# Kernel tuning notes

Measured on AMD Instinct MI355X. Metric: run time of the kernel, lower is better.

Reference implementation:

```python
import jax, jax.numpy as jnp
import numpy as np

INPUT_DIM = 20000
UNITS = 4096
NNZ = 800000
BATCH = 1024


def setup_inputs() -> dict:
    key = jax.random.key(0)
    k1, k2, k3, k4 = jax.random.split(key, 4)
    x = jax.random.normal(k1, (BATCH, INPUT_DIM), dtype=jnp.float32)
    kernel_vector = jax.random.normal(k2, (NNZ,), dtype=jnp.float32) * 0.05
    bias = jnp.zeros((UNITS,), dtype=jnp.float32)
    rows = jax.random.randint(k3, (NNZ,), 0, INPUT_DIM, dtype=jnp.int32)
    cols = jax.random.randint(k4, (NNZ,), 0, UNITS, dtype=jnp.int32)
    nonzero_ind = jnp.stack([rows, cols], axis=1)  # [NNZ, 2]
    return {"x": x, "kernel_vector": kernel_vector, "bias": bias, "nonzero_ind": nonzero_ind}


def reference(x, kernel_vector, bias, nonzero_ind):
    # scatter_nd: build dense (input_dim, units) kernel; duplicates accumulate (matches tf.scatter_nd)
    input_dim = x.shape[1]
    units = bias.shape[0]
    dense_kernel = jnp.zeros((input_dim, units), dtype=kernel_vector.dtype)
    dense_kernel = dense_kernel.at[nonzero_ind[:, 0], nonzero_ind[:, 1]].add(kernel_vector)
    out = jnp.matmul(x, dense_kernel) + bias  # [B, units]
    return jnp.tanh(out)
```

## Files before the change

### kernel.cpp

```cpp
#include <hip/hip_runtime.h>
#include <hip/hip_fp16.h>

#define BATCH      1024
#define INPUT_DIM  20000
#define UNITS      4096
#define NNZ        800000
#define SLOT_CAP   384

#define WS_XT     0
#define WS_CNT    40960000
#define WS_PACKED (WS_CNT + 16384)

__global__ void transpose_in_kernel(const float* __restrict__ x,
                                    unsigned short* __restrict__ xT,
                                    int* __restrict__ cnt) {
    int flat = blockIdx.y * gridDim.x + blockIdx.x;
    int gid = flat * 256 + threadIdx.y * 32 + threadIdx.x;
    if (gid < UNITS) cnt[gid] = 0;

    __shared__ float tile[32][33];
    int d0 = blockIdx.x * 32;
    int b0 = blockIdx.y * 32;
    int tx = threadIdx.x, ty = threadIdx.y;
#pragma unroll
    for (int i = 0; i < 32; i += 8)
        tile[ty + i][tx] = x[(size_t)(b0 + ty + i) * INPUT_DIM + d0 + tx];
    __syncthreads();
#pragma unroll
    for (int i = 0; i < 32; i += 8) {
        __half h = __float2half(tile[tx][ty + i]);
        xT[(size_t)(d0 + ty + i) * BATCH + b0 + tx] = __half_as_ushort(h);
    }
}

__global__ void scatter_kernel(const int* __restrict__ ind, const float* __restrict__ vals,
                               int* __restrict__ cnt, unsigned int* __restrict__ packed) {
    int i = blockIdx.x * blockDim.x + threadIdx.x;
    if (i < NNZ) {
        int r = ind[2 * i];
        int c = ind[2 * i + 1];
        unsigned short hv = __half_as_ushort(__float2half(vals[i]));
        unsigned int e = (unsigned int)r | ((unsigned int)hv << 16);
        int pos = atomicAdd(&cnt[c], 1);
        if (pos < SLOT_CAP) packed[c * SLOT_CAP + pos] = e;
    }
}

__device__ __forceinline__ void acc_one(unsigned int e, const unsigned short* xb,
                                        float& a0, float& a1) {
    unsigned int row = e & 0xFFFFu;
    __half v = __ushort_as_half((unsigned short)(e >> 16));
    unsigned int q = *(const unsigned int*)(xb + ((size_t)row << 10));
    __half2 h = *(__half2*)&q;
    a0 = fmaf(__half2float(__low2half(h)),  __half2float(v), a0);
    a1 = fmaf(__half2float(__high2half(h)), __half2float(v), a1);
}

__global__ __launch_bounds__(512, 8) void spmm_kernel(
    const unsigned int* __restrict__ packed, const int* __restrict__ cnt,
    const unsigned short* __restrict__ xT, const float* __restrict__ bias,
    float* __restrict__ out) {
    __shared__ float tile[128][12];
    int bid = blockIdx.x;
    int kLow = bid & 7;
    int cg = bid >> 3;
    int tid = threadIdx.x;
    int lane = tid & 63;
    int w = __builtin_amdgcn_readfirstlane(tid >> 6);
    int col = (cg << 3) + w;
    int n = cnt[col];
    if (n > SLOT_CAP) n = SLOT_CAP;
    const unsigned int* base = packed + col * SLOT_CAP;
    const unsigned short* xb = xT + (kLow << 7) + (lane << 1);

    float a0 = 0.f, a1 = 0.f;
    int n4 = n & ~3;
    int j = 0;
    for (; j < n4; j += 4) {
        uint4 pp = *(const uint4*)(base + j);
        acc_one(pp.x, xb, a0, a1);
        acc_one(pp.y, xb, a0, a1);
        acc_one(pp.z, xb, a0, a1);
        acc_one(pp.w, xb, a0, a1);
    }
    for (; j < n; ++j)
        acc_one(base[j], xb, a0, a1);

    float bcol = bias[col];
    int r0 = lane << 1;
    tile[r0][w]     = tanhf(a0 + bcol);
    tile[r0 + 1][w] = tanhf(a1 + bcol);
    __syncthreads();

    if (tid < 256) {
        int row = tid >> 1;
        int h = (tid & 1) << 2;
        float4 vv = make_float4(tile[row][h], tile[row][h + 1],
                                tile[row][h + 2], tile[row][h + 3]);
        int b = (kLow << 7) + row;
        *(float4*)(out + (size_t)b * UNITS + (cg << 3) + h) = vv;
    }
}

extern "C" void kernel_launch(void* const* d_in, const int* in_sizes, int n_in,
                              void* d_out, int out_size, void* d_ws, size_t ws_size,
                              hipStream_t stream) {
    const float* x    = (const float*)d_in[0];
    const float* vals = (const float*)d_in[1];
    const float* bias = (const float*)d_in[2];
    const int*   ind  = (const int*)d_in[3];
    float* out = (float*)d_out;

    char* ws = (char*)d_ws;
    unsigned short* xT    = (unsigned short*)(ws + WS_XT);
    int*           cnt    = (int*)(ws + WS_CNT);
    unsigned int*  packed = (unsigned int*)(ws + WS_PACKED);

    transpose_in_kernel<<<dim3(INPUT_DIM / 32, BATCH / 32), dim3(32, 8), 0, stream>>>(x, xT, cnt);
    scatter_kernel<<<NNZ / 256, 256, 0, stream>>>(ind, vals, cnt, packed);
    spmm_kernel<<<4096, 512, 0, stream>>>(packed, cnt, xT, bias, out);
}
```

Measured before the change: 314.9 us.

## Band column lists by row half, process four columns per wave, pack transpose writes

The scatter now splits each column's nonzeros into two row bands, stored as separate offset and fp32 value arrays. Row offsets are precomputed so the SpMM loop only adds a lane offset. The SpMM kernel has each wave handle four columns in turn, visiting all low-band rows before high-band rows so x rows get more cache reuse, and launches fewer blocks with wider output stores. The transpose writes two halves per 32-bit store. Risks are more sequential work per wave, lower parallelism from the smaller grid, and silent truncation if any band slot exceeds the cap of 192.

```diff
diff --git a/kernel.cpp b/kernel.cpp
--- a/kernel.cpp
+++ b/kernel.cpp
@@ -5,101 +5,130 @@
 #define INPUT_DIM  20000
 #define UNITS      4096
 #define NNZ        800000
-#define SLOT_CAP   384
+#define BAND_ROW   10000
+#define CAP        192
+#define NSLOT      (UNITS * 2)
 
-#define WS_XT     0
-#define WS_CNT    40960000
-#define WS_PACKED (WS_CNT + 16384)
+#define WS_XT    0
+#define WS_CNT   40960000
+#define WS_OFFS  (WS_CNT + 32768)
+#define WS_VALS  (WS_OFFS + NSLOT * CAP * 4)
 
-__global__ void transpose_in_kernel(const float* __restrict__ x,
-                                    unsigned short* __restrict__ xT,
-                                    int* __restrict__ cnt) {
+__global__ __launch_bounds__(256) void transpose_in_kernel(
+    const float* __restrict__ x, unsigned int* __restrict__ xTu,
+    int* __restrict__ cnt) {
+    int t = threadIdx.x;
     int flat = blockIdx.y * gridDim.x + blockIdx.x;
-    int gid = flat * 256 + threadIdx.y * 32 + threadIdx.x;
-    if (gid < UNITS) cnt[gid] = 0;
+    int gid = flat * 256 + t;
+    if (gid < NSLOT) cnt[gid] = 0;
 
-    __shared__ float tile[32][33];
+    __shared__ float tile[64][33];
     int d0 = blockIdx.x * 32;
-    int b0 = blockIdx.y * 32;
-    int tx = threadIdx.x, ty = threadIdx.y;
+    int b0 = blockIdx.y * 64;
+    int dl = t & 31;
+    int bl0 = t >> 5;
 #pragma unroll
-    for (int i = 0; i < 32; i += 8)
-        tile[ty + i][tx] = x[(size_t)(b0 + ty + i) * INPUT_DIM + d0 + tx];
+    for (int i = 0; i < 64; i += 8)
+        tile[bl0 + i][dl] = x[(size_t)(b0 + bl0 + i) * INPUT_DIM + d0 + dl];
     __syncthreads();
+    int bp = t & 31;
+    int dl0 = t >> 5;
 #pragma unroll
     for (int i = 0; i < 32; i += 8) {
-        __half h = __float2half(tile[tx][ty + i]);
-        xT[(size_t)(d0 + ty + i) * BATCH + b0 + tx] = __half_as_ushort(h);
+        int d = dl0 + i;
+        unsigned short lo = __half_as_ushort(__float2half(tile[2 * bp][d]));
+        unsigned short hi = __half_as_ushort(__float2half(tile[2 * bp + 1][d]));
+        xTu[(size_t)(d0 + d) * (BATCH / 2) + (b0 >> 1) + bp] =
+            (unsigned int)lo | ((unsigned int)hi << 16);
     }
 }
 
-__global__ void scatter_kernel(const int* __restrict__ ind, const float* __restrict__ vals,
-                               int* __restrict__ cnt, unsigned int* __restrict__ packed) {
+__global__ void scatter_kernel(const int* __restrict__ ind, const float* __restrict__ vals_in,
+                               int* __restrict__ cnt, unsigned int* __restrict__ offs,
+                               float* __restrict__ vals) {
     int i = blockIdx.x * blockDim.x + threadIdx.x;
     if (i < NNZ) {
         int r = ind[2 * i];
         int c = ind[2 * i + 1];
-        unsigned short hv = __half_as_ushort(__float2half(vals[i]));
-        unsigned int e = (unsigned int)r | ((unsigned int)hv << 16);
-        int pos = atomicAdd(&cnt[c], 1);
-        if (pos < SLOT_CAP) packed[c * SLOT_CAP + pos] = e;
+        int band = (r >= BAND_ROW) ? 1 : 0;
+        int slot = (c << 1) + band;
+        int pos = atomicAdd(&cnt[slot], 1);
+        if (pos < CAP) {
+            offs[slot * CAP + pos] = (unsigned int)r << 10;
+            vals[slot * CAP + pos] = vals_in[i];
+        }
     }
 }
 
-__device__ __forceinline__ void acc_one(unsigned int e, const unsigned short* xb,
-                                        float& a0, float& a1) {
-    unsigned int row = e & 0xFFFFu;
-    __half v = __ushort_as_half((unsigned short)(e >> 16));
-    unsigned int q = *(const unsigned int*)(xb + ((size_t)row << 10));
-    __half2 h = *(__half2*)&q;
-    a0 = fmaf(__half2float(__low2half(h)),  __half2float(v), a0);
-    a1 = fmaf(__half2float(__high2half(h)), __half2float(v), a1);
-}
-
 __global__ __launch_bounds__(512, 8) void spmm_kernel(
-    const unsigned int* __restrict__ packed, const int* __restrict__ cnt,
-    const unsigned short* __restrict__ xT, const float* __restrict__ bias,
-    float* __restrict__ out) {
-    __shared__ float tile[128][12];
+    const unsigned int* __restrict__ offs, const float* __restrict__ vals,
+    const int* __restrict__ cnt, const unsigned short* __restrict__ xT,
+    const float* __restrict__ bias, float* __restrict__ out) {
+    __shared__ float tile[128][33];
     int bid = blockIdx.x;
     int kLow = bid & 7;
     int cg = bid >> 3;
     int tid = threadIdx.x;
     int lane = tid & 63;
     int w = __builtin_amdgcn_readfirstlane(tid >> 6);
-    int col = (cg << 3) + w;
-    int n = cnt[col];
-    if (n > SLOT_CAP) n = SLOT_CAP;
-    const unsigned int* base = packed + col * SLOT_CAP;
-    const unsigned short* xb = xT + (kLow << 7) + (lane << 1);
+    int colbase = (cg << 5) + (w << 2);
+    unsigned int laneoff = (unsigned int)(kLow << 7) + (unsigned int)(lane << 1);
 
-    float a0 = 0.f, a1 = 0.f;
-    int n4 = n & ~3;
-    int j = 0;
-    for (; j < n4; j += 4) {
-        uint4 pp = *(const uint4*)(base + j);
-        acc_one(pp.x, xb, a0, a1);
-        acc_one(pp.y, xb, a0, a1);
-        acc_one(pp.z, xb, a0, a1);
-        acc_one(pp.w, xb, a0, a1);
+    float acc[4][2] = {{0.f, 0.f}, {0.f, 0.f}, {0.f, 0.f}, {0.f, 0.f}};
+#pragma unroll
+    for (int bd = 0; bd < 2; ++bd) {
+#pragma unroll
+        for (int c = 0; c < 4; ++c) {
+            int slot = ((colbase + c) << 1) + bd;
+            int n = cnt[slot];
+            if (n > CAP) n = CAP;
+            const unsigned int* ob = offs + slot * CAP;
+            const float* vb = vals + slot * CAP;
+            float a0 = acc[c][0], a1 = acc[c][1];
+            int j = 0;
+            for (; j + 4 <= n; j += 4) {
+                uint4 o4 = *(const uint4*)(ob + j);
+                float4 v4 = *(const float4*)(vb + j);
+                __half2 h0 = *(const __half2*)(xT + (o4.x + laneoff));
+                __half2 h1 = *(const __half2*)(xT + (o4.y + laneoff));
+                __half2 h2 = *(const __half2*)(xT + (o4.z + laneoff));
+                __half2 h3 = *(const __half2*)(xT + (o4.w + laneoff));
+                a0 = fmaf(__half2float(__low2half(h0)),  v4.x, a0);
+                a1 = fmaf(__half2float(__high2half(h0)), v4.x, a1);
+                a0 = fmaf(__half2float(__low2half(h1)),  v4.y, a0);
+                a1 = fmaf(__half2float(__high2half(h1)), v4.y, a1);
+                a0 = fmaf(__half2float(__low2half(h2)),  v4.z, a0);
+                a1 = fmaf(__half2float(__high2half(h2)), v4.z, a1);
+                a0 = fmaf(__half2float(__low2half(h3)),  v4.w, a0);
+                a1 = fmaf(__half2float(__high2half(h3)), v4.w, a1);
+            }
+            for (; j < n; ++j) {
+                __half2 h = *(const __half2*)(xT + (ob[j] + laneoff));
+                float v = vb[j];
+                a0 = fmaf(__half2float(__low2half(h)),  v, a0);
+                a1 = fmaf(__half2float(__high2half(h)), v, a1);
+            }
+            acc[c][0] = a0; acc[c][1] = a1;
+        }
     }
-    for (; j < n; ++j)
-        acc_one(base[j], xb, a0, a1);
 
-    float bcol = bias[col];
     int r0 = lane << 1;
-    tile[r0][w]     = tanhf(a0 + bcol);
-    tile[r0 + 1][w] = tanhf(a1 + bcol);
+#pragma unroll
+    for (int c = 0; c < 4; ++c) {
+        float bc = bias[colbase + c];
+        tile[r0][(w << 2) + c]     = tanhf(acc[c][0] + bc);
+        tile[r0 + 1][(w << 2) + c] = tanhf(acc[c][1] + bc);
+    }
     __syncthreads();
-
-    if (tid < 256) {
-        int row = tid >> 1;
-        int h = (tid & 1) << 2;
-        float4 vv = make_float4(tile[row][h], tile[row][h + 1],
-                                tile[row][h + 2], tile[row][h + 3]);
-        int b = (kLow << 7) + row;
-        *(float4*)(out + (size_t)b * UNITS + (cg << 3) + h) = vv;
-    }
+    int bl = tid >> 2;
+    int c0 = (tid & 3) << 3;
+    float4 u0 = make_float4(tile[bl][c0],     tile[bl][c0 + 1],
+                            tile[bl][c0 + 2], tile[bl][c0 + 3]);
+    float4 u1 = make_float4(tile[bl][c0 + 4], tile[bl][c0 + 5],
+                            tile[bl][c0 + 6], tile[bl][c0 + 7]);
+    size_t obase = (size_t)((kLow << 7) + bl) * UNITS + (cg << 5) + c0;
+    *(float4*)(out + obase)     = u0;
+    *(float4*)(out + obase + 4) = u1;
 }
 
 extern "C" void kernel_launch(void* const* d_in, const int* in_sizes, int n_in,
@@ -112,11 +141,13 @@
     float* out = (float*)d_out;
 
     char* ws = (char*)d_ws;
-    unsigned short* xT    = (unsigned short*)(ws + WS_XT);
-    int*           cnt    = (int*)(ws + WS_CNT);
-    unsigned int*  packed = (unsigned int*)(ws + WS_PACKED);
+    unsigned short* xT  = (unsigned short*)(ws + WS_XT);
+    int*          cnt   = (int*)(ws + WS_CNT);
+    unsigned int* offsA = (unsigned int*)(ws + WS_OFFS);
+    float*        valsA = (float*)(ws + WS_VALS);
 
-    transpose_in_kernel<<<dim3(INPUT_DIM / 32, BATCH / 32), dim3(32, 8), 0, stream>>>(x, xT, cnt);
-    scatter_kernel<<<NNZ / 256, 256, 0, stream>>>(ind, vals, cnt, packed);
-    spmm_kernel<<<4096, 512, 0, stream>>>(packed, cnt, xT, bias, out);
+    transpose_in_kernel<<<dim3(INPUT_DIM / 32, BATCH / 64), 256, 0, stream>>>(
+        x, (unsigned int*)xT, cnt);
+    scatter_kernel<<<NNZ / 256, 256, 0, stream>>>(ind, vals, cnt, offsA, valsA);
+    spmm_kernel<<<1024, 512, 0, stream>>>(offsA, valsA, cnt, xT, bias, out);
 }
```

After: 307.7 us. 2.3% less time.
